# Kernel tuning notes

Measured on AMD Instinct MI355X. Metric: run time of the kernel, lower is better.

Reference implementation:

```python
import jax, jax.numpy as jnp
import numpy as np

D_MODEL = 1024
D_KEY = 64
BATCH = 4
SEQ = 4096


def setup_inputs() -> dict:
    key = jax.random.key(0)
    kq, kk, kv, kwq, kwk, kwv = jax.random.split(key, 6)
    queries = jax.random.normal(kq, (BATCH, SEQ, D_MODEL), dtype=jnp.float32)
    keys = jax.random.normal(kk, (BATCH, SEQ, D_MODEL), dtype=jnp.float32)
    values = jax.random.normal(kv, (BATCH, SEQ, D_MODEL), dtype=jnp.float32)
    # causal mask: 1 = keep, 0 = masked out (torch masked_fill where mask==0)
    mask = jnp.tril(jnp.ones((SEQ, SEQ), dtype=jnp.int32))
    s = 1.0 / np.sqrt(D_MODEL)
    Wq = jax.random.normal(kwq, (D_MODEL, D_KEY), dtype=jnp.float32) * s
    Wk = jax.random.normal(kwk, (D_MODEL, D_KEY), dtype=jnp.float32) * s
    Wv = jax.random.normal(kwv, (D_MODEL, D_KEY), dtype=jnp.float32) * s
    return {"queries": queries, "keys": keys, "values": values,
            "mask": mask, "Wq": Wq, "Wk": Wk, "Wv": Wv}


def reference(queries, keys, values, mask, Wq, Wk, Wv):
    q = jnp.einsum('bsd,dk->bsk', queries, Wq)   # [B,S,dk]
    k = jnp.einsum('bsd,dk->bsk', keys, Wk)
    v = jnp.einsum('bsd,dk->bsk', values, Wv)
    scale = 1.0 / np.sqrt(D_KEY).astype(np.float32)
    attn = jnp.einsum('bqk,bsk->bqs', q, k) * scale  # [B,Sq,Sk]
    attn = jnp.where(mask == 0, -jnp.inf, attn)
    attn = jax.nn.softmax(attn, axis=-1)
    return jnp.einsum('bqs,bsk->bqk', attn, v)      # [B,S,dk]
```

## Files before the change

kernel.cpp:

```cpp
#include <hip/hip_runtime.h>
#include <hip/hip_bf16.h>

#define B      4
#define SEQ    4096
#define DM     1024
#define DK     64
#define NSPLIT 8

typedef __bf16 bf16x8 __attribute__((ext_vector_type(8)));
typedef __bf16 bf16x4 __attribute__((ext_vector_type(4)));
typedef float  f32x4  __attribute__((ext_vector_type(4)));

#define KSTR 72

#define QSCALE 0.1803368801111204f
#define M2BIAS 12.0f

__device__ __forceinline__ void gl_lds16(const void* g, void* l)
{
    __builtin_amdgcn_global_load_lds(
        (const __attribute__((address_space(1))) void*)g,
        (__attribute__((address_space(3))) void*)l, 16, 0, 0);
}

__global__ __launch_bounds__(256) void wt_kernel(
    const float* __restrict__ Wq, const float* __restrict__ Wk,
    const float* __restrict__ Wv, __bf16* __restrict__ Wt)
{
    const int mat = blockIdx.y;
    const float* W = (mat == 0) ? Wq : (mat == 1) ? Wk : Wv;
    const float scale = (mat == 0) ? QSCALE : 1.0f;
    const int k0 = blockIdx.x * 64;
    const int tid = threadIdx.x;

    __shared__ float t[64][65];

    const int r = tid >> 2;
    const int c = (tid & 3) * 16;
    {
        const float* src = W + (size_t)(k0 + r) * DK + c;
        #pragma unroll
        for (int j = 0; j < 4; ++j) {
            float4 a = *(const float4*)(src + j * 4);
            t[r][c + j * 4 + 0] = a.x; t[r][c + j * 4 + 1] = a.y;
            t[r][c + j * 4 + 2] = a.z; t[r][c + j * 4 + 3] = a.w;
        }
    }
    __syncthreads();
    const int n  = tid >> 2;
    const int kk = (tid & 3) * 16;
    bf16x8 b0, b1;
    #pragma unroll
    for (int j = 0; j < 8; ++j) b0[j] = (__bf16)(t[kk + j][n] * scale);
    #pragma unroll
    for (int j = 0; j < 8; ++j) b1[j] = (__bf16)(t[kk + 8 + j][n] * scale);
    __bf16* dst = Wt + (size_t)(mat * DK + n) * DM + k0 + kk;
    *(bf16x8*)(dst)     = b0;
    *(bf16x8*)(dst + 8) = b1;
}

#define NC 32
#define PF 3
__global__ __launch_bounds__(256) void proj_lds_kernel(
    const float* __restrict__ q_in, const float* __restrict__ k_in,
    const float* __restrict__ v_in, const __bf16* __restrict__ Wt,
    __bf16* __restrict__ qb, __bf16* __restrict__ kb,
    __bf16* __restrict__ vtb)
{
    const int m = blockIdx.y;
    const float* in = (m == 0) ? q_in : (m == 1) ? k_in : v_in;
    const __bf16* wt = Wt + (size_t)m * DK * DM;

    const int rowbase = blockIdx.x * 64;
    const int tid  = threadIdx.x;
    const int w    = tid >> 6;
    const int lane = tid & 63;
    const int quad = lane >> 4;
    const int l15  = lane & 15;

    __shared__ float  As[4][64 * 32];
    __shared__ __bf16 Ws[4][64 * 32];

    const int lr = lane >> 3, lu = lane & 7;
    const float* asrc0 = in + (size_t)(rowbase + (w * 2 + 0) * 8 + lr) * DM
                            + ((lu ^ lr) << 2);
    const float* asrc1 = in + (size_t)(rowbase + (w * 2 + 1) * 8 + lr) * DM
                            + ((lu ^ lr) << 2);
    const int wn = lane >> 2, wu = lane & 3;
    const __bf16* wsrc = wt + (size_t)(w * 16 + wn) * DM
                            + (((wu ^ (wn & 3))) << 3);

    auto stage = [&](int c) {
        const int b = c & 3;
        gl_lds16(asrc0 + c * 32, &As[b][(w * 2 + 0) * 256]);
        gl_lds16(asrc1 + c * 32, &As[b][(w * 2 + 1) * 256]);
        gl_lds16(wsrc  + c * 32, &Ws[b][w * 512]);
    };

    f32x4 acc[4];
    #pragma unroll
    for (int nf = 0; nf < 4; ++nf) acc[nf] = (f32x4){0.f, 0.f, 0.f, 0.f};

    stage(0); stage(1); stage(2);

    const int rowl = w * 16 + l15;
    const int h7 = l15 & 7;
    const int h3 = l15 & 3;

    #pragma unroll
    for (int c = 0; c < NC; ++c) {
        if (c == NC - 1)          asm volatile("s_waitcnt vmcnt(0)" ::: "memory");
        else if (c == NC - 2)     asm volatile("s_waitcnt vmcnt(3)" ::: "memory");
        else                      asm volatile("s_waitcnt vmcnt(6)" ::: "memory");
        __builtin_amdgcn_s_barrier();
        __builtin_amdgcn_sched_barrier(0);
        if (c + PF < NC) stage(c + PF);
        const int b = c & 3;
        float4 a0 = *(const float4*)&As[b][rowl * 32 + (((quad * 2)     ^ h7) << 2)];
        float4 a1 = *(const float4*)&As[b][rowl * 32 + (((quad * 2 + 1) ^ h7) << 2)];
        bf16x8 af;
        af[0] = (__bf16)a0.x; af[1] = (__bf16)a0.y;
        af[2] = (__bf16)a0.z; af[3] = (__bf16)a0.w;
        af[4] = (__bf16)a1.x; af[5] = (__bf16)a1.y;
        af[6] = (__bf16)a1.z; af[7] = (__bf16)a1.w;
        #pragma unroll
        for (int nf = 0; nf < 4; ++nf) {
            const int n = nf * 16 + l15;
            bf16x8 wf = *(const bf16x8*)&Ws[b][n * 32 + ((quad ^ h3) << 3)];
            acc[nf] = __builtin_amdgcn_mfma_f32_16x16x32_bf16(af, wf, acc[nf], 0, 0, 0);
        }
    }

    if (m < 2) {
        __bf16* outb = (m == 0) ? qb : kb;
        #pragma unroll
        for (int nf = 0; nf < 4; ++nf)
            #pragma unroll
            for (int r = 0; r < 4; ++r)
                outb[(size_t)(rowbase + w * 16 + quad * 4 + r) * DK + nf * 16 + l15] =
                    (__bf16)acc[nf][r];
    } else {
        const int bb = rowbase >> 12;
        const int s0 = (rowbase & (SEQ - 1)) + w * 16 + quad * 4;
        #pragma unroll
        for (int nf = 0; nf < 4; ++nf) {
            bf16x4 v4;
            #pragma unroll
            for (int r = 0; r < 4; ++r) v4[r] = (__bf16)acc[nf][r];
            *(bf16x4*)&vtb[(size_t)(bb * DK + nf * 16 + l15) * SEQ + s0] = v4;
        }
    }
}

__global__ __launch_bounds__(256) void flash_kernel(
    const __bf16* __restrict__ qb, const __bf16* __restrict__ kb,
    const __bf16* __restrict__ vtb, __bf16* __restrict__ Opart,
    float* __restrict__ lpart)
{
    const int qt  = blockIdx.x;
    const int bb  = blockIdx.y;
    const int z   = blockIdx.z;
    const int tid = threadIdx.x;
    const int w    = tid >> 6;
    const int lane = tid & 63;
    const int quad = lane >> 4;
    const int l15  = lane & 15;

    __shared__ __bf16 Ks[64 * KSTR];
    __shared__ __bf16 Vs[64 * KSTR];
    __shared__ __bf16 Ps[4][2][16 * KSTR];

    const int qrow_base = qt * 128 + w * 32;
    const int niters = 2 * qt + 2;
    const int kt0 = (niters * z) / NSPLIT;
    const int kt1 = (niters * (z + 1)) / NSPLIT;

    bf16x8 qf[2][2];
    #pragma unroll
    for (int g = 0; g < 2; ++g) {
        const __bf16* qp = qb + ((size_t)(bb * SEQ + qrow_base + g * 16 + l15)) * DK + quad * 8;
        qf[g][0] = *(const bf16x8*)(qp);
        qf[g][1] = *(const bf16x8*)(qp + 32);
    }

    bf16x8 ones;
    #pragma unroll
    for (int j = 0; j < 8; ++j) ones[j] = (__bf16)1.0f;

    f32x4 of[2][4], lacc[2];
    #pragma unroll
    for (int g = 0; g < 2; ++g) {
        #pragma unroll
        for (int nf = 0; nf < 4; ++nf) of[g][nf] = (f32x4){0.f, 0.f, 0.f, 0.f};
        lacc[g] = (f32x4){0.f, 0.f, 0.f, 0.f};
    }

    const int sr = tid >> 2;
    const int sc = (tid & 3) * 16;
    bf16x8 kr0, kr1, vr0, vr1;
    const __bf16* kbase = kb  + ((size_t)(bb * SEQ + sr)) * DK + sc;
    const __bf16* vbase = vtb + ((size_t)(bb * DK  + sr)) * SEQ + sc;

    if (kt1 > kt0) {
        const __bf16* kg = kbase + (size_t)kt0 * 64 * DK;
        kr0 = *(const bf16x8*)(kg); kr1 = *(const bf16x8*)(kg + 8);
        const __bf16* vg = vbase + kt0 * 64;
        vr0 = *(const bf16x8*)(vg); vr1 = *(const bf16x8*)(vg + 8);
    }

    for (int kt = kt0; kt < kt1; ++kt) {
        __syncthreads();
        *(bf16x8*)&Ks[sr * KSTR + sc]     = kr0;
        *(bf16x8*)&Ks[sr * KSTR + sc + 8] = kr1;
        *(bf16x8*)&Vs[sr * KSTR + sc]     = vr0;
        *(bf16x8*)&Vs[sr * KSTR + sc + 8] = vr1;
        __syncthreads();
        if (kt + 1 < kt1) {
            const __bf16* kg = kbase + (size_t)(kt + 1) * 64 * DK;
            kr0 = *(const bf16x8*)(kg); kr1 = *(const bf16x8*)(kg + 8);
            const __bf16* vg = vbase + (kt + 1) * 64;
            vr0 = *(const bf16x8*)(vg); vr1 = *(const bf16x8*)(vg + 8);
        }

        f32x4 sf[2][4];
        #pragma unroll
        for (int g = 0; g < 2; ++g)
            #pragma unroll
            for (int nf = 0; nf < 4; ++nf)
                sf[g][nf] = (f32x4){-M2BIAS, -M2BIAS, -M2BIAS, -M2BIAS};
        #pragma unroll
        for (int nf = 0; nf < 4; ++nf) {
            #pragma unroll
            for (int ch = 0; ch < 2; ++ch) {
                bf16x8 kf = *(const bf16x8*)(&Ks[(nf * 16 + l15) * KSTR + ch * 32 + quad * 8]);
                sf[0][nf] = __builtin_amdgcn_mfma_f32_16x16x32_bf16(qf[0][ch], kf, sf[0][nf], 0, 0, 0);
                sf[1][nf] = __builtin_amdgcn_mfma_f32_16x16x32_bf16(qf[1][ch], kf, sf[1][nf], 0, 0, 0);
            }
        }

        const int kc0 = kt * 64;
        #pragma unroll
        for (int g = 0; g < 2; ++g) {
            const int r0 = qrow_base + g * 16;
            const bool dg = (kc0 + 63 > r0);
            #pragma unroll
            for (int nf = 0; nf < 4; ++nf) {
                #pragma unroll
                for (int r = 0; r < 4; ++r) {
                    float s = sf[g][nf][r];
                    if (dg) {
                        const int col = kc0 + nf * 16 + l15;
                        const int row = r0 + quad * 4 + r;
                        if (col > row) s = -1.0e9f;
                    }
                    const float p = __builtin_amdgcn_exp2f(s);
                    Ps[w][g][(quad * 4 + r) * KSTR + nf * 16 + l15] = (__bf16)p;
                }
            }
        }

        bf16x8 pf[2][2];
        #pragma unroll
        for (int g = 0; g < 2; ++g) {
            pf[g][0] = *(const bf16x8*)(&Ps[w][g][l15 * KSTR + quad * 8]);
            pf[g][1] = *(const bf16x8*)(&Ps[w][g][l15 * KSTR + 32 + quad * 8]);
            lacc[g] = __builtin_amdgcn_mfma_f32_16x16x32_bf16(pf[g][0], ones, lacc[g], 0, 0, 0);
            lacc[g] = __builtin_amdgcn_mfma_f32_16x16x32_bf16(pf[g][1], ones, lacc[g], 0, 0, 0);
        }

        #pragma unroll
        for (int nf = 0; nf < 4; ++nf) {
            #pragma unroll
            for (int ch = 0; ch < 2; ++ch) {
                bf16x8 vf = *(const bf16x8*)(&Vs[(nf * 16 + l15) * KSTR + ch * 32 + quad * 8]);
                of[0][nf] = __builtin_amdgcn_mfma_f32_16x16x32_bf16(pf[0][ch], vf, of[0][nf], 0, 0, 0);
                of[1][nf] = __builtin_amdgcn_mfma_f32_16x16x32_bf16(pf[1][ch], vf, of[1][nf], 0, 0, 0);
            }
        }
    }

    #pragma unroll
    for (int g = 0; g < 2; ++g) {
        __bf16* Op = Opart + ((size_t)(z * B + bb) * SEQ + qrow_base + g * 16) * DK;
        #pragma unroll
        for (int nf = 0; nf < 4; ++nf)
            #pragma unroll
            for (int r = 0; r < 4; ++r)
                Op[(size_t)(quad * 4 + r) * DK + nf * 16 + l15] = (__bf16)of[g][nf][r];
        if (l15 == 0) {
            const size_t base = (size_t)(z * B + bb) * SEQ + qrow_base + g * 16 + quad * 4;
            #pragma unroll
            for (int r = 0; r < 4; ++r)
                lpart[base + r] = lacc[g][r];
        }
    }
}

__global__ __launch_bounds__(256) void combine_kernel(
    const __bf16* __restrict__ Opart, const float* __restrict__ lpart,
    float* __restrict__ out)
{
    const int idx = blockIdx.x * 256 + threadIdx.x;
    const int row = idx >> 6;

    float L = 0.f, o = 0.f;
    #pragma unroll
    for (int z = 0; z < NSPLIT; ++z) {
        L += lpart[(size_t)z * (B * SEQ) + row];
        o += (float)Opart[(size_t)z * (B * SEQ) * DK + idx];
    }
    out[idx] = o / L;
}

extern "C" void kernel_launch(void* const* d_in, const int* in_sizes, int n_in,
                              void* d_out, int out_size, void* d_ws, size_t ws_size,
                              hipStream_t stream)
{
    const float* queries = (const float*)d_in[0];
    const float* keys    = (const float*)d_in[1];
    const float* values  = (const float*)d_in[2];
    const float* Wq = (const float*)d_in[4];
    const float* Wk = (const float*)d_in[5];
    const float* Wv = (const float*)d_in[6];
    float* out = (float*)d_out;

    char* p = (char*)d_ws;
    __bf16* qb  = (__bf16*)p;  p += (size_t)B * SEQ * DK * 2;
    __bf16* kb  = (__bf16*)p;  p += (size_t)B * SEQ * DK * 2;
    __bf16* vtb = (__bf16*)p;  p += (size_t)B * SEQ * DK * 2;
    __bf16* Wt  = (__bf16*)p;  p += (size_t)3 * DK * DM * 2;
    __bf16* Opart = (__bf16*)p; p += (size_t)NSPLIT * B * SEQ * DK * 2;
    float* lpart = (float*)p;   p += (size_t)NSPLIT * B * SEQ * 4;

    wt_kernel<<<dim3(DM / 64, 3), 256, 0, stream>>>(Wq, Wk, Wv, Wt);

    proj_lds_kernel<<<dim3((B * SEQ) / 64, 3), 256, 0, stream>>>(
        queries, keys, values, Wt, qb, kb, vtb);

    flash_kernel<<<dim3(SEQ / 128, B, NSPLIT), 256, 0, stream>>>(
        qb, kb, vtb, Opart, lpart);

    combine_kernel<<<(B * SEQ * DK) / 256, 256, 0, stream>>>(
        Opart, lpart, out);
}
```

Baseline: 289.4 us.

## Halve projection row tile to 32 and split N across warps with 3-stage pipeline

The projection kernel now handles 32 rows per block instead of 64, so the grid is twice as large. Each warp computes a 16-row by 32-column quadrant rather than a full 16x64 strip. The LDS ring shrinks from 4 to 3 buffers with prefetch depth 2, and launch bounds request 6 blocks per SM. The aim is higher occupancy and more blocks in flight for this memory-bound fp32 input read, at the cost of loading the weight tile twice as often and a shallower prefetch.

```diff
diff --git a/kernel.cpp b/kernel.cpp
--- a/kernel.cpp
+++ b/kernel.cpp
@@ -60,8 +60,7 @@
 }
 
 #define NC 32
-#define PF 3
-__global__ __launch_bounds__(256) void proj_lds_kernel(
+__global__ __launch_bounds__(256, 6) void proj_lds_kernel(
     const float* __restrict__ q_in, const float* __restrict__ k_in,
     const float* __restrict__ v_in, const __bf16* __restrict__ Wt,
     __bf16* __restrict__ qb, __bf16* __restrict__ kb,
@@ -71,51 +70,49 @@
     const float* in = (m == 0) ? q_in : (m == 1) ? k_in : v_in;
     const __bf16* wt = Wt + (size_t)m * DK * DM;
 
-    const int rowbase = blockIdx.x * 64;
+    const int rowbase = blockIdx.x * 32;
     const int tid  = threadIdx.x;
     const int w    = tid >> 6;
     const int lane = tid & 63;
     const int quad = lane >> 4;
     const int l15  = lane & 15;
-
-    __shared__ float  As[4][64 * 32];
-    __shared__ __bf16 Ws[4][64 * 32];
+    const int band = w & 1;
+    const int nfh  = w >> 1;
+
+    __shared__ float  As[3][32 * 32];
+    __shared__ __bf16 Ws[3][64 * 32];
 
     const int lr = lane >> 3, lu = lane & 7;
-    const float* asrc0 = in + (size_t)(rowbase + (w * 2 + 0) * 8 + lr) * DM
-                            + ((lu ^ lr) << 2);
-    const float* asrc1 = in + (size_t)(rowbase + (w * 2 + 1) * 8 + lr) * DM
-                            + ((lu ^ lr) << 2);
+    const float* asrc = in + (size_t)(rowbase + w * 8 + lr) * DM
+                           + ((lu ^ lr) << 2);
     const int wn = lane >> 2, wu = lane & 3;
     const __bf16* wsrc = wt + (size_t)(w * 16 + wn) * DM
-                            + (((wu ^ (wn & 3))) << 3);
+                            + ((wu ^ (wn & 3)) << 3);
 
     auto stage = [&](int c) {
-        const int b = c & 3;
-        gl_lds16(asrc0 + c * 32, &As[b][(w * 2 + 0) * 256]);
-        gl_lds16(asrc1 + c * 32, &As[b][(w * 2 + 1) * 256]);
-        gl_lds16(wsrc  + c * 32, &Ws[b][w * 512]);
+        const int b = c % 3;
+        gl_lds16(asrc + c * 32, &As[b][w * 256]);
+        gl_lds16(wsrc + c * 32, &Ws[b][w * 512]);
     };
 
-    f32x4 acc[4];
-    #pragma unroll
-    for (int nf = 0; nf < 4; ++nf) acc[nf] = (f32x4){0.f, 0.f, 0.f, 0.f};
-
-    stage(0); stage(1); stage(2);
-
-    const int rowl = w * 16 + l15;
+    f32x4 acc[2];
+    acc[0] = (f32x4){0.f, 0.f, 0.f, 0.f};
+    acc[1] = (f32x4){0.f, 0.f, 0.f, 0.f};
+
+    stage(0); stage(1);
+
+    const int rowl = band * 16 + l15;
     const int h7 = l15 & 7;
     const int h3 = l15 & 3;
 
     #pragma unroll
     for (int c = 0; c < NC; ++c) {
-        if (c == NC - 1)          asm volatile("s_waitcnt vmcnt(0)" ::: "memory");
-        else if (c == NC - 2)     asm volatile("s_waitcnt vmcnt(3)" ::: "memory");
-        else                      asm volatile("s_waitcnt vmcnt(6)" ::: "memory");
+        if (c == NC - 1)  asm volatile("s_waitcnt vmcnt(0)" ::: "memory");
+        else              asm volatile("s_waitcnt vmcnt(2)" ::: "memory");
         __builtin_amdgcn_s_barrier();
         __builtin_amdgcn_sched_barrier(0);
-        if (c + PF < NC) stage(c + PF);
-        const int b = c & 3;
+        if (c + 2 < NC) stage(c + 2);
+        const int b = c % 3;
         float4 a0 = *(const float4*)&As[b][rowl * 32 + (((quad * 2)     ^ h7) << 2)];
         float4 a1 = *(const float4*)&As[b][rowl * 32 + (((quad * 2 + 1) ^ h7) << 2)];
         bf16x8 af;
@@ -124,30 +121,30 @@
         af[4] = (__bf16)a1.x; af[5] = (__bf16)a1.y;
         af[6] = (__bf16)a1.z; af[7] = (__bf16)a1.w;
         #pragma unroll
-        for (int nf = 0; nf < 4; ++nf) {
-            const int n = nf * 16 + l15;
+        for (int j = 0; j < 2; ++j) {
+            const int n = (nfh * 2 + j) * 16 + l15;
             bf16x8 wf = *(const bf16x8*)&Ws[b][n * 32 + ((quad ^ h3) << 3)];
-            acc[nf] = __builtin_amdgcn_mfma_f32_16x16x32_bf16(af, wf, acc[nf], 0, 0, 0);
+            acc[j] = __builtin_amdgcn_mfma_f32_16x16x32_bf16(af, wf, acc[j], 0, 0, 0);
         }
     }
 
     if (m < 2) {
         __bf16* outb = (m == 0) ? qb : kb;
         #pragma unroll
-        for (int nf = 0; nf < 4; ++nf)
+        for (int j = 0; j < 2; ++j)
             #pragma unroll
             for (int r = 0; r < 4; ++r)
-                outb[(size_t)(rowbase + w * 16 + quad * 4 + r) * DK + nf * 16 + l15] =
-                    (__bf16)acc[nf][r];
+                outb[(size_t)(rowbase + band * 16 + quad * 4 + r) * DK
+                     + (nfh * 2 + j) * 16 + l15] = (__bf16)acc[j][r];
     } else {
         const int bb = rowbase >> 12;
-        const int s0 = (rowbase & (SEQ - 1)) + w * 16 + quad * 4;
-        #pragma unroll
-        for (int nf = 0; nf < 4; ++nf) {
+        const int s0 = (rowbase & (SEQ - 1)) + band * 16 + quad * 4;
+        #pragma unroll
+        for (int j = 0; j < 2; ++j) {
             bf16x4 v4;
             #pragma unroll
-            for (int r = 0; r < 4; ++r) v4[r] = (__bf16)acc[nf][r];
-            *(bf16x4*)&vtb[(size_t)(bb * DK + nf * 16 + l15) * SEQ + s0] = v4;
+            for (int r = 0; r < 4; ++r) v4[r] = (__bf16)acc[j][r];
+            *(bf16x4*)&vtb[(size_t)(bb * DK + (nfh * 2 + j) * 16 + l15) * SEQ + s0] = v4;
         }
     }
 }
@@ -334,7 +331,7 @@
 
     wt_kernel<<<dim3(DM / 64, 3), 256, 0, stream>>>(Wq, Wk, Wv, Wt);
 
-    proj_lds_kernel<<<dim3((B * SEQ) / 64, 3), 256, 0, stream>>>(
+    proj_lds_kernel<<<dim3((B * SEQ) / 32, 3), 256, 0, stream>>>(
         queries, keys, values, Wt, qb, kb, vtb);
 
     flash_kernel<<<dim3(SEQ / 128, B, NSPLIT), 256, 0, stream>>>(
```

Measured after the change: 282.3 us. 1.03x faster.

## Load projection activations straight to registers and vectorize the combine kernel

Applied to the files above, without the earlier changes.

The projection kernel no longer stages the fp32 activation tile through LDS. Each lane now loads its own row fragment directly into registers, keeping eight chunks in flight, while only the bf16 weights still go through a 4-deep LDS ring. The vmcnt waits are hand-tuned to fit the new mix of loads, which cuts LDS traffic and shared memory use but makes the global reads less coalesced (each lane reads 32 bytes from a separate row) and raises register pressure. The combine kernel now handles four outputs per thread using vector loads and stores, and multiplies by a reciprocal instead of dividing.

```diff
diff --git a/kernel.cpp b/kernel.cpp
--- a/kernel.cpp
+++ b/kernel.cpp
@@ -59,9 +59,7 @@
     *(bf16x8*)(dst + 8) = b1;
 }
 
-#define NC 32
-#define PF 3
-__global__ __launch_bounds__(256) void proj_lds_kernel(
+__global__ __launch_bounds__(256) void proj_kernel(
     const float* __restrict__ q_in, const float* __restrict__ k_in,
     const float* __restrict__ v_in, const __bf16* __restrict__ Wt,
     __bf16* __restrict__ qb, __bf16* __restrict__ kb,
@@ -78,59 +76,72 @@
     const int quad = lane >> 4;
     const int l15  = lane & 15;
 
-    __shared__ float  As[4][64 * 32];
     __shared__ __bf16 Ws[4][64 * 32];
 
-    const int lr = lane >> 3, lu = lane & 7;
-    const float* asrc0 = in + (size_t)(rowbase + (w * 2 + 0) * 8 + lr) * DM
-                            + ((lu ^ lr) << 2);
-    const float* asrc1 = in + (size_t)(rowbase + (w * 2 + 1) * 8 + lr) * DM
-                            + ((lu ^ lr) << 2);
     const int wn = lane >> 2, wu = lane & 3;
     const __bf16* wsrc = wt + (size_t)(w * 16 + wn) * DM
-                            + (((wu ^ (wn & 3))) << 3);
-
-    auto stage = [&](int c) {
-        const int b = c & 3;
-        gl_lds16(asrc0 + c * 32, &As[b][(w * 2 + 0) * 256]);
-        gl_lds16(asrc1 + c * 32, &As[b][(w * 2 + 1) * 256]);
-        gl_lds16(wsrc  + c * 32, &Ws[b][w * 512]);
-    };
-
-    f32x4 acc[4];
-    #pragma unroll
-    for (int nf = 0; nf < 4; ++nf) acc[nf] = (f32x4){0.f, 0.f, 0.f, 0.f};
-
-    stage(0); stage(1); stage(2);
-
-    const int rowl = w * 16 + l15;
-    const int h7 = l15 & 7;
+                            + ((wu ^ (wn & 3)) << 3);
+    const float* arow = in + (size_t)(rowbase + w * 16 + l15) * DM + quad * 8;
     const int h3 = l15 & 3;
 
-    #pragma unroll
-    for (int c = 0; c < NC; ++c) {
-        if (c == NC - 1)          asm volatile("s_waitcnt vmcnt(0)" ::: "memory");
-        else if (c == NC - 2)     asm volatile("s_waitcnt vmcnt(3)" ::: "memory");
-        else                      asm volatile("s_waitcnt vmcnt(6)" ::: "memory");
-        __builtin_amdgcn_s_barrier();
-        __builtin_amdgcn_sched_barrier(0);
-        if (c + PF < NC) stage(c + PF);
-        const int b = c & 3;
-        float4 a0 = *(const float4*)&As[b][rowl * 32 + (((quad * 2)     ^ h7) << 2)];
-        float4 a1 = *(const float4*)&As[b][rowl * 32 + (((quad * 2 + 1) ^ h7) << 2)];
-        bf16x8 af;
-        af[0] = (__bf16)a0.x; af[1] = (__bf16)a0.y;
-        af[2] = (__bf16)a0.z; af[3] = (__bf16)a0.w;
-        af[4] = (__bf16)a1.x; af[5] = (__bf16)a1.y;
-        af[6] = (__bf16)a1.z; af[7] = (__bf16)a1.w;
-        #pragma unroll
-        for (int nf = 0; nf < 4; ++nf) {
-            const int n = nf * 16 + l15;
-            bf16x8 wf = *(const bf16x8*)&Ws[b][n * 32 + ((quad ^ h3) << 3)];
-            acc[nf] = __builtin_amdgcn_mfma_f32_16x16x32_bf16(af, wf, acc[nf], 0, 0, 0);
-        }
-    }
-
+    gl_lds16(wsrc + 0 * 32, &Ws[0][w * 512]);
+    gl_lds16(wsrc + 1 * 32, &Ws[1][w * 512]);
+    gl_lds16(wsrc + 2 * 32, &Ws[2][w * 512]);
+    __builtin_amdgcn_sched_barrier(0);
+    float4 a0 = *(const float4*)(arow + 0 * 32), b0 = *(const float4*)(arow + 0 * 32 + 4);
+    float4 a1 = *(const float4*)(arow + 1 * 32), b1 = *(const float4*)(arow + 1 * 32 + 4);
+    float4 a2 = *(const float4*)(arow + 2 * 32), b2 = *(const float4*)(arow + 2 * 32 + 4);
+    float4 a3 = *(const float4*)(arow + 3 * 32), b3 = *(const float4*)(arow + 3 * 32 + 4);
+    float4 a4 = *(const float4*)(arow + 4 * 32), b4 = *(const float4*)(arow + 4 * 32 + 4);
+    float4 a5 = *(const float4*)(arow + 5 * 32), b5 = *(const float4*)(arow + 5 * 32 + 4);
+    float4 a6 = *(const float4*)(arow + 6 * 32), b6 = *(const float4*)(arow + 6 * 32 + 4);
+    float4 a7 = *(const float4*)(arow + 7 * 32), b7 = *(const float4*)(arow + 7 * 32 + 4);
+
+    f32x4 acc0 = (f32x4){0.f, 0.f, 0.f, 0.f};
+    f32x4 acc1 = (f32x4){0.f, 0.f, 0.f, 0.f};
+    f32x4 acc2 = (f32x4){0.f, 0.f, 0.f, 0.f};
+    f32x4 acc3 = (f32x4){0.f, 0.f, 0.f, 0.f};
+
+#define CHUNK(c, s, N) do {                                                    \
+    asm volatile("s_waitcnt vmcnt(" #N ")" ::: "memory");                      \
+    __builtin_amdgcn_s_barrier();                                              \
+    __builtin_amdgcn_sched_barrier(0);                                         \
+    if ((c) + 3 < 32)                                                          \
+        gl_lds16(wsrc + ((c) + 3) * 32, &Ws[((c) + 3) & 3][w * 512]);          \
+    bf16x8 af;                                                                 \
+    af[0] = (__bf16)a##s.x; af[1] = (__bf16)a##s.y;                            \
+    af[2] = (__bf16)a##s.z; af[3] = (__bf16)a##s.w;                            \
+    af[4] = (__bf16)b##s.x; af[5] = (__bf16)b##s.y;                            \
+    af[6] = (__bf16)b##s.z; af[7] = (__bf16)b##s.w;                            \
+    {                                                                          \
+        const __bf16* wb = &Ws[(c) & 3][0];                                    \
+        bf16x8 wf0 = *(const bf16x8*)&wb[(0 * 16 + l15) * 32 + ((quad ^ h3) << 3)]; \
+        bf16x8 wf1 = *(const bf16x8*)&wb[(1 * 16 + l15) * 32 + ((quad ^ h3) << 3)]; \
+        bf16x8 wf2 = *(const bf16x8*)&wb[(2 * 16 + l15) * 32 + ((quad ^ h3) << 3)]; \
+        bf16x8 wf3 = *(const bf16x8*)&wb[(3 * 16 + l15) * 32 + ((quad ^ h3) << 3)]; \
+        acc0 = __builtin_amdgcn_mfma_f32_16x16x32_bf16(af, wf0, acc0, 0, 0, 0); \
+        acc1 = __builtin_amdgcn_mfma_f32_16x16x32_bf16(af, wf1, acc1, 0, 0, 0); \
+        acc2 = __builtin_amdgcn_mfma_f32_16x16x32_bf16(af, wf2, acc2, 0, 0, 0); \
+        acc3 = __builtin_amdgcn_mfma_f32_16x16x32_bf16(af, wf3, acc3, 0, 0, 0); \
+    }                                                                          \
+    __builtin_amdgcn_sched_barrier(0);                                         \
+    if ((c) + 8 < 32) {                                                        \
+        a##s = *(const float4*)(arow + ((c) + 8) * 32);                        \
+        b##s = *(const float4*)(arow + ((c) + 8) * 32 + 4);                    \
+    }                                                                          \
+} while (0)
+
+    CHUNK( 0, 0, 8); CHUNK( 1, 1, 8); CHUNK( 2, 2, 8); CHUNK( 3, 3, 8);
+    CHUNK( 4, 4, 8); CHUNK( 5, 5, 8); CHUNK( 6, 6, 8); CHUNK( 7, 7, 8);
+    CHUNK( 8, 0, 8); CHUNK( 9, 1, 8); CHUNK(10, 2, 8); CHUNK(11, 3, 8);
+    CHUNK(12, 4, 8); CHUNK(13, 5, 8); CHUNK(14, 6, 8); CHUNK(15, 7, 8);
+    CHUNK(16, 0, 8); CHUNK(17, 1, 8); CHUNK(18, 2, 8); CHUNK(19, 3, 8);
+    CHUNK(20, 4, 8); CHUNK(21, 5, 8); CHUNK(22, 6, 8); CHUNK(23, 7, 8);
+    CHUNK(24, 0, 8); CHUNK(25, 1, 6); CHUNK(26, 2, 4); CHUNK(27, 3, 2);
+    CHUNK(28, 4, 2); CHUNK(29, 5, 2); CHUNK(30, 6, 1); CHUNK(31, 7, 0);
+#undef CHUNK
+
+    f32x4 accs[4] = {acc0, acc1, acc2, acc3};
     if (m < 2) {
         __bf16* outb = (m == 0) ? qb : kb;
         #pragma unroll
@@ -138,7 +149,7 @@
             #pragma unroll
             for (int r = 0; r < 4; ++r)
                 outb[(size_t)(rowbase + w * 16 + quad * 4 + r) * DK + nf * 16 + l15] =
-                    (__bf16)acc[nf][r];
+                    (__bf16)accs[nf][r];
     } else {
         const int bb = rowbase >> 12;
         const int s0 = (rowbase & (SEQ - 1)) + w * 16 + quad * 4;
@@ -146,7 +157,7 @@
         for (int nf = 0; nf < 4; ++nf) {
             bf16x4 v4;
             #pragma unroll
-            for (int r = 0; r < 4; ++r) v4[r] = (__bf16)acc[nf][r];
+            for (int r = 0; r < 4; ++r) v4[r] = (__bf16)accs[nf][r];
             *(bf16x4*)&vtb[(size_t)(bb * DK + nf * 16 + l15) * SEQ + s0] = v4;
         }
     }
@@ -300,16 +311,20 @@
     const __bf16* __restrict__ Opart, const float* __restrict__ lpart,
     float* __restrict__ out)
 {
-    const int idx = blockIdx.x * 256 + threadIdx.x;
+    const int idx = (blockIdx.x * 256 + threadIdx.x) * 4;
     const int row = idx >> 6;
 
-    float L = 0.f, o = 0.f;
+    float L = 0.f;
+    float o0 = 0.f, o1 = 0.f, o2 = 0.f, o3 = 0.f;
     #pragma unroll
     for (int z = 0; z < NSPLIT; ++z) {
         L += lpart[(size_t)z * (B * SEQ) + row];
-        o += (float)Opart[(size_t)z * (B * SEQ) * DK + idx];
-    }
-    out[idx] = o / L;
+        bf16x4 v = *(const bf16x4*)&Opart[(size_t)z * (B * SEQ) * DK + idx];
+        o0 += (float)v[0]; o1 += (float)v[1]; o2 += (float)v[2]; o3 += (float)v[3];
+    }
+    const float inv = 1.0f / L;
+    float4 res; res.x = o0 * inv; res.y = o1 * inv; res.z = o2 * inv; res.w = o3 * inv;
+    *(float4*)&out[idx] = res;
 }
 
 extern "C" void kernel_launch(void* const* d_in, const int* in_sizes, int n_in,
@@ -334,12 +349,12 @@
 
     wt_kernel<<<dim3(DM / 64, 3), 256, 0, stream>>>(Wq, Wk, Wv, Wt);
 
-    proj_lds_kernel<<<dim3((B * SEQ) / 64, 3), 256, 0, stream>>>(
+    proj_kernel<<<dim3((B * SEQ) / 64, 3), 256, 0, stream>>>(
         queries, keys, values, Wt, qb, kb, vtb);
 
     flash_kernel<<<dim3(SEQ / 128, B, NSPLIT), 256, 0, stream>>>(
         qb, kb, vtb, Opart, lpart);
 
-    combine_kernel<<<(B * SEQ * DK) / 256, 256, 0, stream>>>(
+    combine_kernel<<<(B * SEQ * DK) / 1024, 256, 0, stream>>>(
         Opart, lpart, out);
 }
```

Result: faster. 275.9 us (-4.6%).
